# Kernel optimization log

Hardware: AMD Instinct MI355X
Metric: run time of the kernel (lower is better)

Reference implementation:

```python
import jax, jax.numpy as jnp
import numpy as np

B, N, C = 2, 2048, 1024
H = 16
R = 4
MLP = 4096
LORA_SCALE = 1.0 / R  # lora_alpha=1, r=4
EPS = 1e-5


def _ln(x, g, b):
    m = jnp.mean(x, axis=-1, keepdims=True)
    v = jnp.mean(jnp.square(x - m), axis=-1, keepdims=True)
    return (x - m) * jax.lax.rsqrt(v + EPS) * g + b


def setup_inputs() -> dict:
    key = jax.random.key(0)
    ks = jax.random.split(key, 16)
    s = lambda k, shape, fan: jax.random.normal(k, shape, jnp.float32) * (1.0 / np.sqrt(fan))
    return {
        "x": jax.random.normal(ks[0], (B, N, C), jnp.float32),
        "pos": jax.random.normal(ks[1], (B, N, C), jnp.float32),
        "Wqkv": s(ks[2], (3 * C, C), C),
        "b_qkv": jnp.zeros((3 * C,), jnp.float32),
        "lora_A": s(ks[3], (2 * R, C), C),          # rows 0:R -> q, R:2R -> v
        "lora_B": s(ks[4], (2 * C, R), R) * 0.1,     # rows 0:C -> q, C:2C -> v
        "Wproj": s(ks[5], (C, C), C),
        "b_proj": jnp.zeros((C,), jnp.float32),
        "ln1_g": jnp.ones((C,), jnp.float32),
        "ln1_b": jnp.zeros((C,), jnp.float32),
        "ln2_g": jnp.ones((C,), jnp.float32),
        "ln2_b": jnp.zeros((C,), jnp.float32),
        "W1": s(ks[6], (MLP, C), C),
        "b1": jnp.zeros((MLP,), jnp.float32),
        "W2": s(ks[7], (C, MLP), MLP),
        "b2": jnp.zeros((C,), jnp.float32),
        "idx": 0,
    }


def reference(x, pos, Wqkv, b_qkv, lora_A, lora_B, Wproj, b_proj,
              ln1_g, ln1_b, ln2_g, ln2_b, W1, b1, W2, b2, idx):
    # (dropout layers are identity in eval mode)
    x = x + pos

    # --- attention block: Residual(PreNormDrop(SelfAttention)) ---
    h = _ln(x, ln1_g, ln1_b)                              # [B,N,C]
    qkv = h @ Wqkv.T + b_qkv                              # [B,N,3C]
    # LoRA MergedLinear: low-rank update on q and v thirds only
    after_A = h @ lora_A.T                                # [B,N,2R]
    dq = after_A[..., :R] @ lora_B[:C].T * LORA_SCALE     # [B,N,C]
    dv = after_A[..., R:] @ lora_B[C:].T * LORA_SCALE     # [B,N,C]
    qkv = qkv.at[..., :C].add(dq).at[..., 2 * C:].add(dv)

    Dh = C // H
    q, k, v = [t.reshape(B, N, H, Dh).transpose(0, 2, 1, 3)
               for t in jnp.split(qkv, 3, axis=-1)]       # each [B,H,N,Dh]
    scale = Dh ** -0.5
    attn = jnp.einsum('bhid,bhjd->bhij', q, k) * scale    # [B,H,N,N]
    attn = jax.nn.softmax(attn, axis=-1)
    o = jnp.einsum('bhij,bhjd->bhid', attn, v)            # [B,H,N,Dh]
    o = o.transpose(0, 2, 1, 3).reshape(B, N, C)
    o = o @ Wproj.T + b_proj
    x = x + o

    # --- FFN block: Residual(PreNorm(FeedForward)) ---
    h2 = _ln(x, ln2_g, ln2_b)
    h2 = jax.nn.gelu(h2 @ W1.T + b1, approximate=False)
    h2 = h2 @ W2.T + b2
    return x + h2
```

## Files before the change

kernel.cpp:

```cpp
#include <hip/hip_runtime.h>
#include <hip/hip_bf16.h>
#include <math.h>

typedef __hip_bfloat16 bf16;
typedef __attribute__((ext_vector_type(4))) float f32x4;
typedef __attribute__((ext_vector_type(16))) float f32x16;
typedef __attribute__((ext_vector_type(8))) short s16x8;

__device__ __forceinline__ void async_cp16(void* lds, const void* g) {
    __builtin_amdgcn_global_load_lds((const __attribute__((address_space(1))) void*)g,
                                     (__attribute__((address_space(3))) void*)lds, 16, 0, 0);
}

__device__ __forceinline__ float gelu_fast(float x) {
    float y = 1.5957691216f * (x + 0.044715f * x * x * x);
    float t = __expf(y);
    float th = 1.0f - 2.0f / (t + 1.0f);
    return 0.5f * x * (1.0f + th);
}

__global__ __launch_bounds__(256)
void cvt_all(const float* __restrict__ w0, const float* __restrict__ w1,
             const float* __restrict__ w2, const float* __restrict__ w3,
             bf16* __restrict__ o0, bf16* __restrict__ o1,
             bf16* __restrict__ o2, bf16* __restrict__ o3) {
    int i = blockIdx.x * 256 + threadIdx.x;
    const float* src; bf16* dst; int j = i;
    if (j < 786432)            { src = w0; dst = o0; }
    else if (j < 1048576)      { j -= 786432;  src = w1; dst = o1; }
    else if (j < 2097152)      { j -= 1048576; src = w2; dst = o2; }
    else                       { j -= 2097152; src = w3; dst = o3; }
    float4 v = ((const float4*)src)[j];
    union { bf16 o[4]; uint2 u; } pk;
    pk.o[0] = __float2bfloat16(v.x); pk.o[1] = __float2bfloat16(v.y);
    pk.o[2] = __float2bfloat16(v.z); pk.o[3] = __float2bfloat16(v.w);
    ((uint2*)dst)[j] = pk.u;
}

template <bool ADD>
__global__ __launch_bounds__(256)
void ln_kernel(const float* __restrict__ xin, const float* __restrict__ pos,
               const float* __restrict__ gam, const float* __restrict__ bet,
               float* __restrict__ x1, bf16* __restrict__ hout) {
    const int row = blockIdx.x, tid = threadIdx.x;
    const size_t off = (size_t)row * 1024;
    float4 v = ((const float4*)(xin + off))[tid];
    if constexpr (ADD) {
        float4 p = ((const float4*)(pos + off))[tid];
        v.x += p.x; v.y += p.y; v.z += p.z; v.w += p.w;
        ((float4*)(x1 + off))[tid] = v;
    }
    float s  = v.x + v.y + v.z + v.w;
    float s2 = v.x*v.x + v.y*v.y + v.z*v.z + v.w*v.w;
#pragma unroll
    for (int o = 32; o >= 1; o >>= 1) { s += __shfl_xor(s, o); s2 += __shfl_xor(s2, o); }
    __shared__ float sS[4], sS2[4];
    int w = tid >> 6, lane = tid & 63;
    if (lane == 0) { sS[w] = s; sS2[w] = s2; }
    __syncthreads();
    float mean = (sS[0] + sS[1] + sS[2] + sS[3]) * (1.f / 1024.f);
    float e2   = (sS2[0] + sS2[1] + sS2[2] + sS2[3]) * (1.f / 1024.f);
    float rstd = rsqrtf(e2 - mean * mean + 1e-5f);
    float4 gv = ((const float4*)gam)[tid], bv = ((const float4*)bet)[tid];
    bf16* ho = hout + off + tid * 4;
    ho[0] = __float2bfloat16((v.x - mean) * rstd * gv.x + bv.x);
    ho[1] = __float2bfloat16((v.y - mean) * rstd * gv.y + bv.y);
    ho[2] = __float2bfloat16((v.z - mean) * rstd * gv.z + bv.z);
    ho[3] = __float2bfloat16((v.w - mean) * rstd * gv.w + bv.w);
}

template <int MODE>
__global__ __launch_bounds__(256)
void gemm_bk64(const bf16* __restrict__ A, const bf16* __restrict__ B,
               const float* __restrict__ bias, bf16* __restrict__ outp,
               int M, int N, int K, int gx) {
    __shared__ bf16 As[2][128 * 64];
    __shared__ bf16 Bs[2][128 * 64];
    const int tid = threadIdx.x;
    const int lane = tid & 63, w = tid >> 6;
    const int grp = lane >> 4, c16 = lane & 15;
    const int wm = (w & 1) * 64, wn = (w >> 1) * 64;
    const int nwg = gridDim.x, bid = blockIdx.x;
    const int sw = (bid & 7) * (nwg >> 3) + (bid >> 3);
    const int bm = (sw / gx) * 128, bn = (sw % gx) * 128;

    f32x4 acc[4][4];
    const f32x4 zero = {0.f, 0.f, 0.f, 0.f};
#pragma unroll
    for (int mi = 0; mi < 4; mi++)
#pragma unroll
        for (int ni = 0; ni < 4; ni++) acc[mi][ni] = zero;

#define STAGE128(bufi, k0)                                                          \
    {                                                                               \
        const int buf_ = (bufi);                                                    \
        const int koff_ = (k0);                                                     \
        _Pragma("unroll") for (int t_ = 0; t_ < 4; t_++) {                          \
            int s_ = t_ * 256 + tid;                                                \
            int row_ = s_ >> 3, db_ = s_ & 7;                                       \
            int gb_ = (db_ ^ (row_ & 7)) << 3;                                      \
            async_cp16(&As[buf_][s_ * 8], A + (size_t)(bm + row_) * K + koff_ + gb_); \
            async_cp16(&Bs[buf_][s_ * 8], B + (size_t)(bn + row_) * K + koff_ + gb_); \
        }                                                                           \
    }

#define COMPUTE128(bufi)                                                            \
    {                                                                               \
        const int buf_ = (bufi);                                                    \
        _Pragma("unroll") for (int kc_ = 0; kc_ < 2; kc_++) {                       \
            s16x8 af_[4], bfv_[4];                                                  \
            _Pragma("unroll") for (int mi_ = 0; mi_ < 4; mi_++) {                   \
                int r_ = wm + mi_ * 16 + c16;                                       \
                af_[mi_] = *(const s16x8*)&As[buf_][r_ * 64 + ((((kc_ << 2) | grp) ^ (r_ & 7)) << 3)]; \
            }                                                                       \
            _Pragma("unroll") for (int ni_ = 0; ni_ < 4; ni_++) {                   \
                int r_ = wn + ni_ * 16 + c16;                                       \
                bfv_[ni_] = *(const s16x8*)&Bs[buf_][r_ * 64 + ((((kc_ << 2) | grp) ^ (r_ & 7)) << 3)]; \
            }                                                                       \
            _Pragma("unroll") for (int mi_ = 0; mi_ < 4; mi_++)                     \
                _Pragma("unroll") for (int ni_ = 0; ni_ < 4; ni_++)                 \
                    acc[mi_][ni_] = __builtin_amdgcn_mfma_f32_16x16x32_bf16(af_[mi_], bfv_[ni_], acc[mi_][ni_], 0, 0, 0); \
        }                                                                           \
    }

    STAGE128(0, 0);
    __syncthreads();
    const int nk = K >> 6;
    int cur = 0;
    for (int t = 0; t < nk - 1; t++) {
        STAGE128(cur ^ 1, (t + 1) << 6);
        COMPUTE128(cur);
        __syncthreads();
        cur ^= 1;
    }
    COMPUTE128(cur);

#undef STAGE128
#undef COMPUTE128

#pragma unroll
    for (int mi = 0; mi < 4; mi++)
#pragma unroll
        for (int ni = 0; ni < 4; ni++) {
            int r0 = bm + wm + mi * 16 + grp * 4;
            int c  = bn + wn + ni * 16 + c16;
            float bv = bias[c];
#pragma unroll
            for (int q = 0; q < 4; q++) {
                size_t idx = (size_t)(r0 + q) * N + c;
                float v = acc[mi][ni][q] + bv;
                if constexpr (MODE == 2) v = gelu_fast(v);
                outp[idx] = __float2bfloat16(v);
            }
        }
}

__global__ __launch_bounds__(256)
void gemm_n64(const bf16* __restrict__ A, const bf16* __restrict__ B,
              const float* __restrict__ bias, const float* __restrict__ resid,
              float* __restrict__ outp, int M, int N, int K, int gx) {
    __shared__ bf16 As[2][128 * 64];
    __shared__ bf16 Bs[2][64 * 64];
    const int tid = threadIdx.x;
    const int lane = tid & 63, w = tid >> 6;
    const int grp = lane >> 4, c16 = lane & 15;
    const int wm = w * 32;
    const int nwg = gridDim.x, bid = blockIdx.x;
    const int sw = (bid & 7) * (nwg >> 3) + (bid >> 3);
    const int bm = (sw / gx) * 128, bn = (sw % gx) * 64;

    f32x4 acc[2][4];
    const f32x4 zero = {0.f, 0.f, 0.f, 0.f};
#pragma unroll
    for (int mi = 0; mi < 2; mi++)
#pragma unroll
        for (int ni = 0; ni < 4; ni++) acc[mi][ni] = zero;

#define STAGE64(bufi, k0)                                                           \
    {                                                                               \
        const int buf_ = (bufi);                                                    \
        const int koff_ = (k0);                                                     \
        _Pragma("unroll") for (int t_ = 0; t_ < 4; t_++) {                          \
            int s_ = t_ * 256 + tid;                                                \
            int row_ = s_ >> 3, db_ = s_ & 7;                                       \
            async_cp16(&As[buf_][s_ * 8], A + (size_t)(bm + row_) * K + koff_ + ((db_ ^ (row_ & 7)) << 3)); \
        }                                                                           \
        _Pragma("unroll") for (int t_ = 0; t_ < 2; t_++) {                          \
            int s_ = t_ * 256 + tid;                                                \
            int row_ = s_ >> 3, db_ = s_ & 7;                                       \
            async_cp16(&Bs[buf_][s_ * 8], B + (size_t)(bn + row_) * K + koff_ + ((db_ ^ (row_ & 7)) << 3)); \
        }                                                                           \
    }

#define COMPUTE64(bufi)                                                             \
    {                                                                               \
        const int buf_ = (bufi);                                                    \
        _Pragma("unroll") for (int kc_ = 0; kc_ < 2; kc_++) {                       \
            s16x8 af_[2], bfv_[4];                                                  \
            _Pragma("unroll") for (int mi_ = 0; mi_ < 2; mi_++) {                   \
                int r_ = wm + mi_ * 16 + c16;                                       \
                af_[mi_] = *(const s16x8*)&As[buf_][r_ * 64 + ((((kc_ << 2) | grp) ^ (r_ & 7)) << 3)]; \
            }                                                                       \
            _Pragma("unroll") for (int ni_ = 0; ni_ < 4; ni_++) {                   \
                int rb_ = ni_ * 16 + c16;                                           \
                bfv_[ni_] = *(const s16x8*)&Bs[buf_][rb_ * 64 + ((((kc_ << 2) | grp) ^ (rb_ & 7)) << 3)]; \
            }                                                                       \
            _Pragma("unroll") for (int mi_ = 0; mi_ < 2; mi_++)                     \
                _Pragma("unroll") for (int ni_ = 0; ni_ < 4; ni_++)                 \
                    acc[mi_][ni_] = __builtin_amdgcn_mfma_f32_16x16x32_bf16(af_[mi_], bfv_[ni_], acc[mi_][ni_], 0, 0, 0); \
        }                                                                           \
    }

    STAGE64(0, 0);
    __syncthreads();
    const int nk = K >> 6;
    int cur = 0;
    for (int t = 0; t < nk - 1; t++) {
        STAGE64(cur ^ 1, (t + 1) << 6);
        COMPUTE64(cur);
        __syncthreads();
        cur ^= 1;
    }
    COMPUTE64(cur);

#undef STAGE64
#undef COMPUTE64

#pragma unroll
    for (int mi = 0; mi < 2; mi++)
#pragma unroll
        for (int ni = 0; ni < 4; ni++) {
            int r0 = bm + wm + mi * 16 + grp * 4;
            int c  = bn + ni * 16 + c16;
            float bv = bias[c];
#pragma unroll
            for (int q = 0; q < 4; q++) {
                size_t idx = (size_t)(r0 + q) * N + c;
                outp[idx] = acc[mi][ni][q] + bv + resid[idx];
            }
        }
}

__global__ __launch_bounds__(256)
void lora_a_kernel(const bf16* __restrict__ h, const float* __restrict__ A,
                   float* __restrict__ afterA) {
    const int row = blockIdx.x, tid = threadIdx.x;
    float hv[4];
#pragma unroll
    for (int t = 0; t < 4; t++) hv[t] = __bfloat162float(h[(size_t)row * 1024 + tid * 4 + t]);
    float p[8];
#pragma unroll
    for (int r = 0; r < 8; r++) {
        float4 av = ((const float4*)(A + (size_t)r * 1024))[tid];
        p[r] = hv[0] * av.x + hv[1] * av.y + hv[2] * av.z + hv[3] * av.w;
    }
#pragma unroll
    for (int r = 0; r < 8; r++)
#pragma unroll
        for (int o = 32; o >= 1; o >>= 1) p[r] += __shfl_xor(p[r], o);
    __shared__ float red[4][8];
    int w = tid >> 6, lane = tid & 63;
    if (lane == 0) {
#pragma unroll
        for (int r = 0; r < 8; r++) red[w][r] = p[r];
    }
    __syncthreads();
    if (tid < 8) afterA[(size_t)row * 8 + tid] = red[0][tid] + red[1][tid] + red[2][tid] + red[3][tid];
}

__global__ __launch_bounds__(256)
void attn_prep(const bf16* __restrict__ qkv, const float* __restrict__ afterA,
               const float* __restrict__ loraB, bf16* __restrict__ Qb,
               bf16* __restrict__ Kb, bf16* __restrict__ Vt) {
    const int bh = blockIdx.y, b = bh >> 4, h = bh & 15;
    const int it = blockIdx.x;
    __shared__ bf16 Vs[64 * 65];
    const int tid = threadIdx.x;
#pragma unroll
    for (int t = 0; t < 16; t++) {
        int s = t * 256 + tid;
        int il = s >> 6, d = s & 63;
        int ig = b * 2048 + it * 64 + il;
        size_t grow = (size_t)ig * 3072 + h * 64 + d;
        int col = h * 64 + d;
        const float* aA = afterA + (size_t)ig * 8;
        float4 bq = ((const float4*)loraB)[col];
        float4 bvv = ((const float4*)loraB)[1024 + col];
        float dq = (aA[0]*bq.x  + aA[1]*bq.y  + aA[2]*bq.z  + aA[3]*bq.w)  * 0.25f;
        float dv = (aA[4]*bvv.x + aA[5]*bvv.y + aA[6]*bvv.z + aA[7]*bvv.w) * 0.25f;
        float q = (__bfloat162float(qkv[grow]) + dq) * 0.18033688011f;
        float k = __bfloat162float(qkv[grow + 1024]);
        float v = __bfloat162float(qkv[grow + 2048]) + dv;
        size_t orow = (size_t)(bh * 2048 + it * 64 + il) * 64 + d;
        Qb[orow] = __float2bfloat16(q);
        Kb[orow] = __float2bfloat16(k);
        Vs[d * 65 + il] = __float2bfloat16(v);
    }
    __syncthreads();
#pragma unroll
    for (int t = 0; t < 16; t++) {
        int s = t * 256 + tid;
        int d = s >> 6, il = s & 63;
        Vt[(size_t)(bh * 64 + d) * 2048 + it * 64 + il] = Vs[d * 65 + il];
    }
}

__global__ __launch_bounds__(256)
void attn_fused(const bf16* __restrict__ Qb, const bf16* __restrict__ Kb,
                const bf16* __restrict__ Vt, bf16* __restrict__ Og) {
    __shared__ bf16 Qs[128 * 64], Ks[2][64 * 64], Vs[2][64 * 64];
    const int tid = threadIdx.x;
    const int lane = tid & 63, w = tid >> 6;
    const int c32 = lane & 31, l5 = lane >> 5;
    const int bid = blockIdx.x;
    const int sw = (bid & 7) * 64 + (bid >> 3);
    const int bh = sw >> 4, b = bh >> 4, h = bh & 15;
    const int i0 = (sw & 15) * 128;
    const int rowperm = (c32 & 19) | (((c32 >> 3) & 1) << 2) | (((c32 >> 2) & 1) << 3);

    const size_t qbase = (size_t)(bh * 2048 + i0) * 64;
    const size_t kbase = (size_t)bh * 2048 * 64;
    const size_t vbase = (size_t)bh * 64 * 2048;

#define STAGEKV(bufi, jv)                                                           \
    {                                                                               \
        const int buf_ = (bufi);                                                    \
        const int joff_ = (jv);                                                     \
        _Pragma("unroll") for (int t_ = 0; t_ < 2; t_++) {                          \
            int s_ = t_ * 256 + tid;                                                \
            int row_ = s_ >> 3, db_ = s_ & 7;                                       \
            int gb_ = (db_ ^ (row_ & 7)) << 3;                                      \
            async_cp16(&Ks[buf_][s_ * 8], Kb + kbase + (size_t)(joff_ + row_) * 64 + gb_); \
            async_cp16(&Vs[buf_][s_ * 8], Vt + vbase + (size_t)row_ * 2048 + joff_ + gb_); \
        }                                                                           \
    }

#pragma unroll
    for (int t = 0; t < 4; t++) {
        int s = t * 256 + tid;
        int row = s >> 3, db = s & 7;
        async_cp16(&Qs[s * 8], Qb + qbase + row * 64 + ((db ^ (row & 7)) << 3));
    }
    STAGEKV(0, 0);
    __syncthreads();

    s16x8 qf[4];
    {
        int rq = w * 32 + c32;
#pragma unroll
        for (int kc = 0; kc < 4; kc++) {
            int db = 2 * kc + l5;
            qf[kc] = *(const s16x8*)&Qs[rq * 64 + ((db ^ (rq & 7)) << 3)];
        }
    }

    f32x16 Oq[2];
#pragma unroll
    for (int dq = 0; dq < 2; dq++)
#pragma unroll
        for (int r = 0; r < 16; r++) Oq[dq][r] = 0.f;
    float l_lane = 0.f;

#define ATILE(BUF, JN)                                                              \
    {                                                                               \
        const int jn_ = (JN);                                                       \
        if (jn_ < 32) { STAGEKV((BUF) ^ 1, jn_ << 6); }                             \
        f32x16 Sq[2];                                                               \
        __builtin_amdgcn_s_setprio(1);                                              \
        _Pragma("unroll") for (int jq_ = 0; jq_ < 2; jq_++) {                       \
            _Pragma("unroll") for (int r_ = 0; r_ < 16; r_++) Sq[jq_][r_] = 0.f;    \
            int rk_ = jq_ * 32 + rowperm;                                           \
            _Pragma("unroll") for (int kc_ = 0; kc_ < 4; kc_++) {                   \
                int db_ = 2 * kc_ + l5;                                             \
                s16x8 af_ = *(const s16x8*)&Ks[BUF][rk_ * 64 + ((db_ ^ (rk_ & 7)) << 3)]; \
                Sq[jq_] = __builtin_amdgcn_mfma_f32_32x32x16_bf16(af_, qf[kc_], Sq[jq_], 0, 0, 0); \
            }                                                                       \
        }                                                                           \
        __builtin_amdgcn_s_setprio(0);                                              \
        s16x8 pf_[4];                                                               \
        _Pragma("unroll") for (int kc_ = 0; kc_ < 4; kc_++) {                       \
            union { s16x8 v; unsigned u4[4]; } u_;                                  \
            _Pragma("unroll") for (int pr_ = 0; pr_ < 4; pr_++) {                   \
                float a_ = Sq[kc_ >> 1][8 * (kc_ & 1) + 2 * pr_];                   \
                float b_ = Sq[kc_ >> 1][8 * (kc_ & 1) + 2 * pr_ + 1];               \
                float pa_, pb_;                                                     \
                asm("v_exp_f32 %0, %1" : "=v"(pa_) : "v"(a_));                      \
                asm("v_exp_f32 %0, %1" : "=v"(pb_) : "v"(b_));                      \
                l_lane += pa_; l_lane += pb_;                                       \
                unsigned pk_;                                                       \
                asm("v_cvt_pk_bf16_f32 %0, %1, %2" : "=v"(pk_) : "v"(pa_), "v"(pb_)); \
                u_.u4[pr_] = pk_;                                                   \
            }                                                                       \
            pf_[kc_] = u_.v;                                                        \
        }                                                                           \
        __builtin_amdgcn_s_setprio(1);                                              \
        _Pragma("unroll") for (int dq_ = 0; dq_ < 2; dq_++) {                       \
            int rd_ = dq_ * 32 + c32;                                               \
            _Pragma("unroll") for (int kc_ = 0; kc_ < 4; kc_++) {                   \
                int jb_ = 2 * kc_ + l5;                                             \
                s16x8 af_ = *(const s16x8*)&Vs[BUF][rd_ * 64 + ((jb_ ^ (rd_ & 7)) << 3)]; \
                Oq[dq_] = __builtin_amdgcn_mfma_f32_32x32x16_bf16(af_, pf_[kc_], Oq[dq_], 0, 0, 0); \
            }                                                                       \
        }                                                                           \
        __builtin_amdgcn_s_setprio(0);                                              \
        __syncthreads();                                                            \
    }

    for (int jt = 0; jt < 32; jt += 2) {
        ATILE(0, jt + 1);
        ATILE(1, jt + 2);
    }
#undef ATILE
#undef STAGEKV

    float l = l_lane + __shfl_xor(l_lane, 32);
    float inv = 1.0f / fmaxf(l, 1e-35f);
    int i = i0 + w * 32 + c32;
    size_t obase = (size_t)(b * 2048 + i) * 1024 + h * 64;
#pragma unroll
    for (int dq = 0; dq < 2; dq++)
#pragma unroll
        for (int rg = 0; rg < 4; rg++) {
            union { bf16 e[4]; uint2 u; } pk;
#pragma unroll
            for (int c = 0; c < 4; c++)
                pk.e[c] = __float2bfloat16(Oq[dq][rg * 4 + c] * inv);
            int d0 = dq * 32 + l5 * 4 + rg * 8;
            *(uint2*)&Og[obase + d0] = pk.u;
        }
}

extern "C" void kernel_launch(void* const* d_in, const int* in_sizes, int n_in,
                              void* d_out, int out_size, void* d_ws, size_t ws_size,
                              hipStream_t stream) {
    const float* x     = (const float*)d_in[0];
    const float* pos   = (const float*)d_in[1];
    const float* Wqkv  = (const float*)d_in[2];
    const float* bqkv  = (const float*)d_in[3];
    const float* loraA = (const float*)d_in[4];
    const float* loraB = (const float*)d_in[5];
    const float* Wproj = (const float*)d_in[6];
    const float* bproj = (const float*)d_in[7];
    const float* ln1g  = (const float*)d_in[8];
    const float* ln1b  = (const float*)d_in[9];
    const float* ln2g  = (const float*)d_in[10];
    const float* ln2b  = (const float*)d_in[11];
    const float* W1    = (const float*)d_in[12];
    const float* b1    = (const float*)d_in[13];
    const float* W2    = (const float*)d_in[14];
    const float* b2    = (const float*)d_in[15];

    char* ws = (char*)d_ws;
    float* x1     = (float*)(ws + 0);
    bf16*  hbuf   = (bf16*) (ws + 16777216);
    bf16*  qkv    = (bf16*) (ws + 25165824);
    bf16*  gbuf   = (bf16*) (ws + 50331648);
    float* afterA = (float*)(ws + 83886080);
    bf16*  Qb     = (bf16*) (ws + 84017152);
    bf16*  Kb     = (bf16*) (ws + 92405760);
    bf16*  Vt     = (bf16*) (ws + 100794368);
    bf16*  Obf    = (bf16*) (ws + 109182976);
    bf16*  Wqkvb  = (bf16*) (ws + 117571584);
    bf16*  Wprojb = (bf16*) (ws + 123863040);
    bf16*  W1b    = (bf16*) (ws + 125960192);
    bf16*  W2b    = (bf16*) (ws + 134348800);

    cvt_all<<<12288, 256, 0, stream>>>(Wqkv, Wproj, W1, W2, Wqkvb, Wprojb, W1b, W2b);

    ln_kernel<true><<<4096, 256, 0, stream>>>(x, pos, ln1g, ln1b, x1, hbuf);

    gemm_bk64<0><<<768, 256, 0, stream>>>(hbuf, Wqkvb, bqkv, qkv, 4096, 3072, 1024, 24);

    lora_a_kernel<<<4096, 256, 0, stream>>>(hbuf, loraA, afterA);

    attn_prep<<<dim3(32, 32), 256, 0, stream>>>(qkv, afterA, loraB, Qb, Kb, Vt);
    attn_fused<<<512, 256, 0, stream>>>(Qb, Kb, Vt, Obf);

    gemm_n64<<<512, 256, 0, stream>>>(Obf, Wprojb, bproj, x1, x1, 4096, 1024, 1024, 16);

    ln_kernel<false><<<4096, 256, 0, stream>>>(x1, nullptr, ln2g, ln2b, nullptr, hbuf);

    gemm_bk64<2><<<1024, 256, 0, stream>>>(hbuf, W1b, b1, gbuf, 4096, 4096, 1024, 32);

    gemm_n64<<<512, 256, 0, stream>>>(gbuf, W2b, b2, x1, (float*)d_out, 4096, 1024, 4096, 16);

    (void)in_sizes; (void)n_in; (void)out_size; (void)ws_size;
}
```

Measured before the change: 404.6 us.

## Triple-buffer gemm_n64 LDS pipeline with explicit vmcnt waits

Moves the N=64 GEMM (projection/FFN-down with residual) from a double buffer to a three-stage LDS pipeline. Global-to-LDS async copies are issued two tiles ahead, and completion is tracked with explicit s_waitcnt vmcnt counts plus raw s_barrier instead of __syncthreads. The aim is to hide more global load latency behind MFMA compute. The cost is 50% more LDS, which may lower occupancy, and the loop logic assumes nk-1 is divisible by 3 and that the vmcnt counts match the loads issued per stage.

```diff
diff --git a/kernel.cpp b/kernel.cpp
--- a/kernel.cpp
+++ b/kernel.cpp
@@ -159,8 +159,8 @@
 void gemm_n64(const bf16* __restrict__ A, const bf16* __restrict__ B,
               const float* __restrict__ bias, const float* __restrict__ resid,
               float* __restrict__ outp, int M, int N, int K, int gx) {
-    __shared__ bf16 As[2][128 * 64];
-    __shared__ bf16 Bs[2][64 * 64];
+    __shared__ bf16 As[3][128 * 64];
+    __shared__ bf16 Bs[3][64 * 64];
     const int tid = threadIdx.x;
     const int lane = tid & 63, w = tid >> 6;
     const int grp = lane >> 4, c16 = lane & 15;
@@ -211,18 +211,39 @@
         }                                                                           \
     }
 
+#define WAITV12 asm volatile("s_waitcnt vmcnt(12)" ::: "memory")
+#define WAITV6  asm volatile("s_waitcnt vmcnt(6)"  ::: "memory")
+#define WAITV0  asm volatile("s_waitcnt vmcnt(0)"  ::: "memory")
+
+#define STEP64(BQ, TQ)                                                              \
+    {                                                                               \
+        const int tq_ = (TQ);                                                       \
+        COMPUTE64(BQ);                                                              \
+        __builtin_amdgcn_s_barrier();            \
+        if (tq_ + 3 < nk) { STAGE64(BQ, (tq_ + 3) << 6); WAITV12; }                 \
+        else if (tq_ + 2 < nk) { WAITV6; }                                          \
+        else { WAITV0; }                                \
+        __builtin_amdgcn_s_barrier();             \
+    }
+
+    const int nk = K >> 6;
     STAGE64(0, 0);
-    __syncthreads();
-    const int nk = K >> 6;
-    int cur = 0;
-    for (int t = 0; t < nk - 1; t++) {
-        STAGE64(cur ^ 1, (t + 1) << 6);
-        COMPUTE64(cur);
-        __syncthreads();
-        cur ^= 1;
-    }
-    COMPUTE64(cur);
-
+    STAGE64(1, 64);
+    STAGE64(2, 128);
+    WAITV12;
+    __builtin_amdgcn_s_barrier();
+
+    for (int t = 0; t < nk - 1; t += 3) {
+        STEP64(0, t);
+        STEP64(1, t + 1);
+        STEP64(2, t + 2);
+    }
+    COMPUTE64(0);
+
+#undef STEP64
+#undef WAITV12
+#undef WAITV6
+#undef WAITV0
 #undef STAGE64
 #undef COMPUTE64
 
```

Result: faster. 383.8 us (-5.1%).
